# Kernel optimization log

Measured on AMD Instinct MI355X. Metric: run time of the kernel, lower is better.

## Reference

```python
import jax, jax.numpy as jnp
import numpy as np

WS = 11
SIGMA = 1.5
CH = 3
C1 = (0.01 * 255.0) ** 2  # 6.5025
C2 = (0.03 * 255.0) ** 2  # 58.5225


def _gauss_window():
    # 1D Gaussian -> outer product -> depthwise kernel [C, 1, ws, ws] (OIHW)
    coords = jnp.arange(WS, dtype=jnp.float32) - WS // 2
    g = jnp.exp(-coords ** 2 / (2.0 * SIGMA ** 2))
    g = g / g.sum()
    w2d = g[:, None] * g[None, :]
    return jnp.tile(w2d[None, None], (CH, 1, 1, 1))


def _dwconv(x, win):
    pad = WS // 2
    return jax.lax.conv_general_dilated(
        x, win, window_strides=(1, 1), padding=[(pad, pad), (pad, pad)],
        feature_group_count=CH,
        dimension_numbers=('NCHW', 'OIHW', 'NCHW'))


def setup_inputs() -> dict:
    key = jax.random.key(0)
    k1, k2 = jax.random.split(key)
    shape = (32, 3, 512, 512)
    img_gen = jax.random.uniform(k1, shape, jnp.float32, -1.0, 1.0)
    img_ref = jax.random.uniform(k2, shape, jnp.float32, -1.0, 1.0)
    return {"img_gen": img_gen, "img_ref": img_ref}


def reference(img_gen, img_ref):
    gen = (img_gen + 1.0) * 0.5
    ref = (img_ref + 1.0) * 0.5
    win = _gauss_window()

    mu1 = _dwconv(gen, win)
    mu2 = _dwconv(ref, win)
    mu1_sq = mu1 * mu1
    mu2_sq = mu2 * mu2
    mu1_mu2 = mu1 * mu2
    sigma1_sq = _dwconv(gen * gen, win) - mu1_sq
    sigma2_sq = _dwconv(ref * ref, win) - mu2_sq
    sigma12 = _dwconv(gen * ref, win) - mu1_mu2

    ssim_map = ((2.0 * mu1_mu2 + C1) * (2.0 * sigma12 + C2)) / (
        (mu1_sq + mu2_sq + C1) * (sigma1_sq + sigma2_sq + C2))
    return 1.0 - ssim_map.mean()
```

## Files before the change

### kernel.cpp

```cpp
#include <hip/hip_runtime.h>

typedef float v2f __attribute__((ext_vector_type(2)));

#define TX 64
#define TY 20
#define MY 2
#define BYR (TY * MY)
#define WIN 30
#define HSTR 65
#define IMW 512
#define IMH 512
#define NPLANES 96
#define NBX (IMW / TX)
#define NBY ((IMH + BYR - 1) / BYR)
#define NBLOCKS (NBX * NBY * NPLANES)

#define GW0 0.00102838f
#define GW1 0.00759877f
#define GW2 0.03600077f
#define GW3 0.10936069f
#define GW4 0.21300553f
#define GW5 0.26601172f

__device__ __forceinline__ void pkfma(v2f& acc, v2f a, v2f b) {
  asm("v_pk_fma_f32 %0, %1, %2, %0" : "+v"(acc) : "v"(a), "v"(b));
}
__device__ __forceinline__ v2f pkmul(v2f a, v2f b) {
  v2f d;
  asm("v_pk_mul_f32 %0, %1, %2" : "=v"(d) : "v"(a), "v"(b));
  return d;
}

struct Raw {
  float4 g[6];
  float4 r[6];
};

__device__ __forceinline__ void hload(
    const float* __restrict__ gp, const float* __restrict__ rp,
    int x0, bool fast, int nrows, int gy0, int tid, Raw& L) {
  if (tid >= nrows * 8) return;
  const int r = tid >> 3;
  const int xs = (tid & 7) * 8;
  const int gy = gy0 + r;
  const int xbase = x0 + xs - 8;
  const float* grow = gp + (size_t)gy * IMW;
  const float* rrow = rp + (size_t)gy * IMW;
  if (fast) {
#pragma unroll
    for (int k = 0; k < 6; ++k) {
      L.g[k] = *(const float4*)(grow + xbase + 4 * k);
      L.r[k] = *(const float4*)(rrow + xbase + 4 * k);
    }
  } else {
    const bool rowok = (gy >= 0) & (gy < IMH);
#pragma unroll
    for (int k = 0; k < 6; ++k) {
      const int c = xbase + 4 * k;
      const bool ok = rowok && (c >= 0) && (c < IMW);
      float4 g4 = make_float4(-1.f, -1.f, -1.f, -1.f);
      float4 r4 = g4;
      if (ok) {
        g4 = *(const float4*)(grow + c);
        r4 = *(const float4*)(rrow + c);
      }
      L.g[k] = g4;
      L.r[k] = r4;
    }
  }
}

__device__ __forceinline__ void hcompute(
    const Raw& L, float* __restrict__ sq, int nrows, int slot0, int tid) {
  if (tid >= nrows * 8) return;
  const float GW[11] = {GW0, GW1, GW2, GW3, GW4, GW5,
                        GW4, GW3, GW2, GW1, GW0};
  const int r = tid >> 3;
  const int xs = (tid & 7) * 8;
  int slot = slot0 + r;
  if (slot >= WIN) slot -= WIN;

  v2f P[24];
#pragma unroll
  for (int k = 0; k < 6; ++k) {
    const float4 g4 = L.g[k];
    const float4 r4 = L.r[k];
    P[4 * k + 0] = (v2f){fmaf(0.5f, g4.x, 0.5f), fmaf(0.5f, r4.x, 0.5f)};
    P[4 * k + 1] = (v2f){fmaf(0.5f, g4.y, 0.5f), fmaf(0.5f, r4.y, 0.5f)};
    P[4 * k + 2] = (v2f){fmaf(0.5f, g4.z, 0.5f), fmaf(0.5f, r4.z, 0.5f)};
    P[4 * k + 3] = (v2f){fmaf(0.5f, g4.w, 0.5f), fmaf(0.5f, r4.w, 0.5f)};
  }

  v2f accP[8], accQ[8];
  float accS[8];
#pragma unroll
  for (int o = 0; o < 8; ++o) {
    accP[o] = (v2f){0.f, 0.f};
    accQ[o] = (v2f){0.f, 0.f};
    accS[o] = 0.f;
  }

#pragma unroll
  for (int p = 0; p < 18; ++p) {
    const v2f pv = P[p + 3];
    const v2f qv = pkmul(pv, pv);
    const float sv = pv.x * pv.y;
    const int olo = (p - 10 < 0) ? 0 : p - 10;
    const int ohi = (p < 7) ? p : 7;
#pragma unroll
    for (int o = olo; o <= ohi; ++o) {
      const float wt = GW[p - o];
      const v2f wv = (v2f){wt, wt};
      pkfma(accP[o], wv, pv);
      pkfma(accQ[o], wv, qv);
      accS[o] = fmaf(wt, sv, accS[o]);
    }
  }

  float* dst = sq + slot * (5 * HSTR) + xs;
#pragma unroll
  for (int o = 0; o < 8; ++o) dst[0 * HSTR + o] = accP[o].x;
#pragma unroll
  for (int o = 0; o < 8; ++o) dst[1 * HSTR + o] = accP[o].y;
#pragma unroll
  for (int o = 0; o < 8; ++o) dst[2 * HSTR + o] = accQ[o].x;
#pragma unroll
  for (int o = 0; o < 8; ++o) dst[3 * HSTR + o] = accQ[o].y;
#pragma unroll
  for (int o = 0; o < 8; ++o) dst[4 * HSTR + o] = accS[o];
}

__device__ __forceinline__ float phase2(
    const float* __restrict__ sq, int winbase, int ybase, int col, int r0) {
  const float GW[11] = {GW0, GW1, GW2, GW3, GW4, GW5,
                        GW4, GW3, GW2, GW1, GW0};
  v2f hp[15], hq[15];
  float hs[15];
#pragma unroll
  for (int i = 0; i < 15; ++i) {
    int slot = winbase + r0 + i;
    if (slot >= WIN) slot -= WIN;
    const float* rowp = sq + slot * (5 * HSTR) + col;
    hp[i] = (v2f){rowp[0 * HSTR], rowp[1 * HSTR]};
    hq[i] = (v2f){rowp[2 * HSTR], rowp[3 * HSTR]};
    hs[i] = rowp[4 * HSTR];
  }

  const float C1 = 6.5025f, C2 = 58.5225f;
  float lsum = 0.f;
#pragma unroll
  for (int o = 0; o < 5; ++o) {
    v2f mu = (v2f){0.f, 0.f};
    v2f ee = (v2f){0.f, 0.f};
    float e12 = 0.f;
#pragma unroll
    for (int t = 0; t < 11; ++t) {
      const float wt = GW[t];
      const v2f wv = (v2f){wt, wt};
      pkfma(mu, wv, hp[o + t]);
      pkfma(ee, wv, hq[o + t]);
      e12 = fmaf(wt, hs[o + t], e12);
    }
    const float mu1 = mu.x, mu2 = mu.y, e1 = ee.x, e2 = ee.y;
    const float m12 = mu1 * mu2;
    const float m1s = mu1 * mu1;
    const float m2s = mu2 * mu2;
    const float num = (2.f * m12 + C1) * (2.f * (e12 - m12) + C2);
    const float den = (m1s + m2s + C1) * ((e1 - m1s) + (e2 - m2s) + C2);
    const int y = ybase + r0 + o;
    lsum += (y < IMH) ? __fdividef(num, den) : 0.f;
  }
  return lsum;
}

__global__ __launch_bounds__(256, 4) void ssim_main(
    const float* __restrict__ gen, const float* __restrict__ ref,
    double* __restrict__ partial) {
  __shared__ float s_q[WIN][5][HSTR];
  __shared__ double swsum[4];
  float* const sq = &s_q[0][0][0];

  const int tid = threadIdx.x;
  const int bid = blockIdx.x;
  const int bx = bid & (NBX - 1);
  const int rem = bid >> 3;
  const int by = rem % NBY;
  const int plane = rem / NBY;
  const int x0 = bx * TX;
  const int Y0 = by * BYR;
  const float* gp = gen + (size_t)plane * (IMW * IMH);
  const float* rp = ref + (size_t)plane * (IMW * IMH);
  const bool ix = (bx >= 1) & (bx <= NBX - 2);

  const int col = tid & 63;
  const int r0 = __builtin_amdgcn_readfirstlane((tid >> 6) * 5);

  Raw L0;
  hload(gp, rp, x0, ix & (Y0 - 5 >= 0) & (Y0 + 25 <= IMH), WIN, Y0 - 5, tid, L0);
  hcompute(L0, sq, WIN, 0, tid);

  Raw L1;
  hload(gp, rp, x0, ix & (Y0 + 45 <= IMH), TY, Y0 + 25, tid, L1);

  __syncthreads();

  double acc = (double)phase2(sq, 0, Y0, col, r0);

  __syncthreads();

  hcompute(L1, sq, TY, 0, tid);

  __syncthreads();

  acc += (double)phase2(sq, 20, Y0 + TY, col, r0);

#pragma unroll
  for (int off = 32; off > 0; off >>= 1) acc += __shfl_down(acc, off, 64);
  if ((tid & 63) == 0) swsum[tid >> 6] = acc;
  __syncthreads();
  if (tid == 0) partial[bid] = swsum[0] + swsum[1] + swsum[2] + swsum[3];
}

__global__ void ssim_reduce(const double* __restrict__ partial,
                            float* __restrict__ out) {
  const int tid = threadIdx.x;
  double s = 0.0;
  for (int i = tid; i < NBLOCKS; i += 256) s += partial[i];
#pragma unroll
  for (int off = 32; off > 0; off >>= 1) s += __shfl_down(s, off, 64);
  __shared__ double sd[4];
  if ((tid & 63) == 0) sd[tid >> 6] = s;
  __syncthreads();
  if (tid == 0) {
    const double npix = (double)NPLANES * (double)IMW * (double)IMH;
    out[0] = (float)(1.0 - (sd[0] + sd[1] + sd[2] + sd[3]) / npix);
  }
}

extern "C" void kernel_launch(void* const* d_in, const int* in_sizes, int n_in,
                              void* d_out, int out_size, void* d_ws, size_t ws_size,
                              hipStream_t stream) {
  (void)in_sizes; (void)n_in; (void)out_size; (void)ws_size;
  const float* gen = (const float*)d_in[0];
  const float* ref = (const float*)d_in[1];
  double* partial = (double*)d_ws;
  ssim_main<<<NBLOCKS, 256, 0, stream>>>(gen, ref, partial);
  ssim_reduce<<<1, 256, 0, stream>>>(partial, (float*)d_out);
}
```

Measured before the change: 278.9 us.

## Stream taller row bands through a ring buffer with double-buffered loads

Each block now covers 64 output rows in eight 8-row chunks instead of 40 rows in two chunks. Horizontal-pass results go into an 18-row ring buffer in shared memory, and global loads for the next chunk are double-buffered so they overlap the vertical pass. This cuts halo recomputation (10 halo rows per 64 instead of per 40) and shrinks LDS use so more blocks fit per CU (launch bounds 6). The cost is more barriers per block and a longer serial loop per block.

```diff
diff --git a/kernel.cpp b/kernel.cpp
--- a/kernel.cpp
+++ b/kernel.cpp
@@ -3,16 +3,16 @@
 typedef float v2f __attribute__((ext_vector_type(2)));
 
 #define TX 64
-#define TY 20
-#define MY 2
+#define TY 8
+#define MY 8
 #define BYR (TY * MY)
-#define WIN 30
+#define WIN 18
 #define HSTR 65
 #define IMW 512
 #define IMH 512
 #define NPLANES 96
 #define NBX (IMW / TX)
-#define NBY ((IMH + BYR - 1) / BYR)
+#define NBY (IMH / BYR)
 #define NBLOCKS (NBX * NBY * NPLANES)
 
 #define GW0 0.00102838f
@@ -131,14 +131,14 @@
 }
 
 __device__ __forceinline__ float phase2(
-    const float* __restrict__ sq, int winbase, int ybase, int col, int r0) {
+    const float* __restrict__ sq, int wb, int col, int r0) {
   const float GW[11] = {GW0, GW1, GW2, GW3, GW4, GW5,
                         GW4, GW3, GW2, GW1, GW0};
-  v2f hp[15], hq[15];
-  float hs[15];
-#pragma unroll
-  for (int i = 0; i < 15; ++i) {
-    int slot = winbase + r0 + i;
+  v2f hp[12], hq[12];
+  float hs[12];
+#pragma unroll
+  for (int i = 0; i < 12; ++i) {
+    int slot = wb + r0 + i;
     if (slot >= WIN) slot -= WIN;
     const float* rowp = sq + slot * (5 * HSTR) + col;
     hp[i] = (v2f){rowp[0 * HSTR], rowp[1 * HSTR]};
@@ -149,7 +149,7 @@
   const float C1 = 6.5025f, C2 = 58.5225f;
   float lsum = 0.f;
 #pragma unroll
-  for (int o = 0; o < 5; ++o) {
+  for (int o = 0; o < 2; ++o) {
     v2f mu = (v2f){0.f, 0.f};
     v2f ee = (v2f){0.f, 0.f};
     float e12 = 0.f;
@@ -167,25 +167,23 @@
     const float m2s = mu2 * mu2;
     const float num = (2.f * m12 + C1) * (2.f * (e12 - m12) + C2);
     const float den = (m1s + m2s + C1) * ((e1 - m1s) + (e2 - m2s) + C2);
-    const int y = ybase + r0 + o;
-    lsum += (y < IMH) ? __fdividef(num, den) : 0.f;
+    lsum += __fdividef(num, den);
   }
   return lsum;
 }
 
-__global__ __launch_bounds__(256, 4) void ssim_main(
+__global__ __launch_bounds__(256, 6) void ssim_main(
     const float* __restrict__ gen, const float* __restrict__ ref,
     double* __restrict__ partial) {
   __shared__ float s_q[WIN][5][HSTR];
-  __shared__ double swsum[4];
   float* const sq = &s_q[0][0][0];
 
   const int tid = threadIdx.x;
   const int bid = blockIdx.x;
   const int bx = bid & (NBX - 1);
   const int rem = bid >> 3;
-  const int by = rem % NBY;
-  const int plane = rem / NBY;
+  const int by = rem & (NBY - 1);
+  const int plane = rem >> 3;
   const int x0 = bx * TX;
   const int Y0 = by * BYR;
   const float* gp = gen + (size_t)plane * (IMW * IMH);
@@ -193,29 +191,38 @@
   const bool ix = (bx >= 1) & (bx <= NBX - 2);
 
   const int col = tid & 63;
-  const int r0 = __builtin_amdgcn_readfirstlane((tid >> 6) * 5);
-
-  Raw L0;
-  hload(gp, rp, x0, ix & (Y0 - 5 >= 0) & (Y0 + 25 <= IMH), WIN, Y0 - 5, tid, L0);
-  hcompute(L0, sq, WIN, 0, tid);
-
-  Raw L1;
-  hload(gp, rp, x0, ix & (Y0 + 45 <= IMH), TY, Y0 + 25, tid, L1);
-
-  __syncthreads();
-
-  double acc = (double)phase2(sq, 0, Y0, col, r0);
-
-  __syncthreads();
-
-  hcompute(L1, sq, TY, 0, tid);
-
-  __syncthreads();
-
-  acc += (double)phase2(sq, 20, Y0 + TY, col, r0);
+  const int r0 = __builtin_amdgcn_readfirstlane((tid >> 6) * 2);
+
+  Raw A, B;
+  hload(gp, rp, x0, ix & (by > 0), WIN, Y0 - 5, tid, A);
+  hcompute(A, sq, WIN, 0, tid);
+  hload(gp, rp, x0, ix, TY, Y0 + 13, tid, B);
+  __syncthreads();
+
+  double acc = 0.0;
+  int wb = 0;
+#pragma unroll 2
+  for (int c = 0; c < MY - 1; ++c) {
+    acc += (double)phase2(sq, wb, col, r0);
+    __syncthreads();
+    if (c & 1) hcompute(A, sq, TY, wb, tid);
+    else       hcompute(B, sq, TY, wb, tid);
+    if (c < MY - 2) {
+      const int gy0 = Y0 + 21 + 8 * c;
+      const bool f = ix && (gy0 + TY <= IMH);
+      if (c & 1) hload(gp, rp, x0, f, TY, gy0, tid, B);
+      else       hload(gp, rp, x0, f, TY, gy0, tid, A);
+    }
+    __syncthreads();
+    wb += TY;
+    if (wb >= WIN) wb -= WIN;
+  }
+  acc += (double)phase2(sq, wb, col, r0);
 
 #pragma unroll
   for (int off = 32; off > 0; off >>= 1) acc += __shfl_down(acc, off, 64);
+  __syncthreads();
+  double* swsum = (double*)sq;
   if ((tid & 63) == 0) swsum[tid >> 6] = acc;
   __syncthreads();
   if (tid == 0) partial[bid] = swsum[0] + swsum[1] + swsum[2] + swsum[3];
```

New measurement: 1.045 ms. 3.75x slower.
